# Optimization experiments

Measured on AMD Instinct MI355X. Metric: run time of the kernel, lower is better.

The kernel has to match this reference:

```python
import jax, jax.numpy as jnp
import numpy as np

EMB_DIM = 1024
K = 512
N = 65536
B = 128
EPS = 1e-8  # torch cosine_similarity eps


def setup_inputs() -> dict:
    key = jax.random.key(0)
    k1, k2, k3, k4 = jax.random.split(key, 4)
    x = jax.random.normal(k1, (B, K, EMB_DIM), dtype=jnp.float32)
    query = jax.random.normal(k2, (EMB_DIM,), dtype=jnp.float32)
    # learned parameters: N separate (1, emb_dim) params, concatenated -> [N, EMB_DIM]
    glorot_std = float(np.sqrt(6.0 / (1 + EMB_DIM)))
    prompts = jax.random.uniform(k3, (N, EMB_DIM), dtype=jnp.float32,
                                 minval=-glorot_std, maxval=glorot_std)
    keys = jax.random.normal(k4, (N, EMB_DIM), dtype=jnp.float32)
    return {"x": x, "query": query, "keys": keys, "prompts": prompts}


def reference(x, query, keys, prompts):
    # cosine similarity between query [D] and each key row [N, D]
    q_norm = jnp.maximum(jnp.linalg.norm(query), EPS)
    k_norms = jnp.maximum(jnp.linalg.norm(keys, axis=1), EPS)  # [N]
    sims = (keys @ query) / (k_norms * q_norm)                 # [N]
    _, topk_idx = jax.lax.top_k(sims, K)                       # [K]
    selected = prompts[topk_idx]                               # [K, D] gather
    return x + selected                                        # broadcast over batch
```

## Files before the change

kernel.cpp:

```cpp
#include <hip/hip_runtime.h>
#include <cfloat>
#include <cstdint>

#define EMB_DIM 1024
#define NKEYS   65536
#define TOPK    512
#define BATCH   128
#define NBINS   4096
#define CAP     2048

__global__ __launch_bounds__(256) void sims_kernel(
    const float* __restrict__ keys, const float* __restrict__ query,
    double* __restrict__ sims)
{
    const int wave = threadIdx.x >> 6;
    const int lane = threadIdx.x & 63;
    const int row  = blockIdx.x * 4 + wave;

    const float4* __restrict__ krow = (const float4*)(keys + (size_t)row * EMB_DIM);
    const float4* __restrict__ q4   = (const float4*)query;

    double dot = 0.0, ss = 0.0;
#pragma unroll
    for (int j = 0; j < 4; ++j) {
        const int c = lane + 64 * j;
        float4 kv = krow[c];
        float4 qv = q4[c];
        dot += (double)kv.x * qv.x + (double)kv.y * qv.y +
               (double)kv.z * qv.z + (double)kv.w * qv.w;
        ss  += (double)kv.x * kv.x + (double)kv.y * kv.y +
               (double)kv.z * kv.z + (double)kv.w * kv.w;
    }
#pragma unroll
    for (int off = 32; off > 0; off >>= 1) {
        dot += __shfl_xor(dot, off);
        ss  += __shfl_xor(ss, off);
    }
    if (lane == 0) {
        double norm = sqrt(ss);
        if (norm < 1e-8) norm = 1e-8;
        sims[row] = dot / norm;
    }
}

__device__ __forceinline__ unsigned mono32(float f) {
    unsigned u = __float_as_uint(f);
    return (u & 0x80000000u) ? ~u : (u | 0x80000000u);
}

__global__ __launch_bounds__(1024) void topk_kernel(
    const double* __restrict__ sims, int* __restrict__ topk)
{
    __shared__ int    hist[NBINS];
    __shared__ int    sfx[NBINS];
    __shared__ double cs[CAP];
    __shared__ int    ci[CAP];
    __shared__ int    bstar_s;
    __shared__ int    cnt;

    const int tid = threadIdx.x;

    for (int i = tid; i < NBINS; i += 1024) hist[i] = 0;
    if (tid == 0) cnt = 0;
    __syncthreads();

    for (int n = tid; n < NKEYS; n += 1024) {
        unsigned b = mono32((float)sims[n]) >> 20;
        atomicAdd(&hist[b], 1);
    }
    __syncthreads();

    int* src = hist;
    int* dst = sfx;
    for (int off = 1; off < NBINS; off <<= 1) {
        for (int i = tid; i < NBINS; i += 1024) {
            int v = src[i];
            if (i + off < NBINS) v += src[i + off];
            dst[i] = v;
        }
        __syncthreads();
        int* t = src; src = dst; dst = t;
    }
    for (int i = tid; i < NBINS; i += 1024) {
        if (src[i] >= TOPK && (i == NBINS - 1 || src[i + 1] < TOPK)) bstar_s = i;
    }
    __syncthreads();
    const int bstar = bstar_s;

    for (int n = tid; n < NKEYS; n += 1024) {
        double s = sims[n];
        unsigned b = mono32((float)s) >> 20;
        if ((int)b >= bstar) {
            int pos = atomicAdd(&cnt, 1);
            if (pos < CAP) { cs[pos] = s; ci[pos] = n; }
        }
    }
    __syncthreads();

    int c = cnt; if (c > CAP) c = CAP;
    for (int i = tid; i < CAP; i += 1024) {
        if (i >= c) { cs[i] = -DBL_MAX; ci[i] = 0x7fffffff; }
    }
    __syncthreads();

    for (int k = 2; k <= CAP; k <<= 1) {
        for (int j = k >> 1; j > 0; j >>= 1) {
            for (int i = tid; i < CAP; i += 1024) {
                int ixj = i ^ j;
                if (ixj > i) {
                    double s1 = cs[i], s2 = cs[ixj];
                    int    i1 = ci[i], i2 = ci[ixj];
                    bool a_after_b = (s1 < s2) || (s1 == s2 && i1 > i2);
                    bool up = ((i & k) == 0);
                    if (up ? a_after_b : !a_after_b) {
                        cs[i] = s2; ci[i] = i2;
                        cs[ixj] = s1; ci[ixj] = i1;
                    }
                }
            }
            __syncthreads();
        }
    }

    if (tid < TOPK) topk[tid] = ci[tid];
}

__global__ __launch_bounds__(256) void add_kernel(
    const float* __restrict__ x, const float* __restrict__ prompts,
    const int* __restrict__ topk, float* __restrict__ out)
{
    const int b = blockIdx.x & (BATCH - 1);
    const int k = blockIdx.x >> 7;
    const int idx = topk[k];

    const size_t row = ((size_t)b * TOPK + k) * (EMB_DIM / 4);
    const float4* __restrict__ xr = (const float4*)x + row;
    const float4* __restrict__ pr = (const float4*)prompts + (size_t)idx * (EMB_DIM / 4);
    float4* __restrict__ outr = (float4*)out + row;

    const int t = threadIdx.x;
    float4 xv = xr[t];
    float4 pv = pr[t];
    outr[t] = make_float4(xv.x + pv.x, xv.y + pv.y, xv.z + pv.z, xv.w + pv.w);
}

extern "C" void kernel_launch(void* const* d_in, const int* in_sizes, int n_in,
                              void* d_out, int out_size, void* d_ws, size_t ws_size,
                              hipStream_t stream)
{
    const float* x       = (const float*)d_in[0];
    const float* query   = (const float*)d_in[1];
    const float* keys    = (const float*)d_in[2];
    const float* prompts = (const float*)d_in[3];

    double* sims = (double*)d_ws;
    int*    topk = (int*)((char*)d_ws + NKEYS * sizeof(double));

    sims_kernel<<<NKEYS / 4, 256, 0, stream>>>(keys, query, sims);
    topk_kernel<<<1, 1024, 0, stream>>>(sims, topk);
    add_kernel<<<BATCH * TOPK, 256, 0, stream>>>(x, prompts, topk, (float*)d_out);
}
```

Before: 763.1 us.

## Split single-block top-k into fused histogram, parallel collect, and rank-based selection

Builds the similarity histogram with global atomics inside the sims kernel instead of a second pass in a single block. The threshold bin is found in a small kernel, candidate collection runs across 64 blocks, and the bitonic sort is replaced by an O(c^2) rank count that writes each winner directly to its position. This targets the serial single-block top-k stage, at the cost of more kernel launches, global atomic contention on the histogram, and quadratic work in the candidate count.

```diff
diff --git a/kernel.cpp b/kernel.cpp
--- a/kernel.cpp
+++ b/kernel.cpp
@@ -9,9 +9,21 @@
 #define NBINS   4096
 #define CAP     2048
 
+__device__ __forceinline__ unsigned mono32(float f) {
+    unsigned u = __float_as_uint(f);
+    return (u & 0x80000000u) ? ~u : (u | 0x80000000u);
+}
+
+__global__ __launch_bounds__(1024) void init_kernel(int* __restrict__ hist)
+{
+#pragma unroll
+    for (int j = 0; j < NBINS / 1024; ++j) hist[threadIdx.x + 1024 * j] = 0;
+    if (threadIdx.x == 0) hist[NBINS] = 0;
+}
+
 __global__ __launch_bounds__(256) void sims_kernel(
     const float* __restrict__ keys, const float* __restrict__ query,
-    double* __restrict__ sims)
+    double* __restrict__ sims, int* __restrict__ hist)
 {
     const int wave = threadIdx.x >> 6;
     const int lane = threadIdx.x & 63;
@@ -39,39 +51,24 @@
     if (lane == 0) {
         double norm = sqrt(ss);
         if (norm < 1e-8) norm = 1e-8;
-        sims[row] = dot / norm;
+        double s = dot / norm;
+        sims[row] = s;
+        atomicAdd(&hist[mono32((float)s) >> 20], 1);
     }
 }
 
-__device__ __forceinline__ unsigned mono32(float f) {
-    unsigned u = __float_as_uint(f);
-    return (u & 0x80000000u) ? ~u : (u | 0x80000000u);
-}
-
-__global__ __launch_bounds__(1024) void topk_kernel(
-    const double* __restrict__ sims, int* __restrict__ topk)
+__global__ __launch_bounds__(1024) void bstar_kernel(
+    const int* __restrict__ hist_g, int* __restrict__ bstar_g)
 {
-    __shared__ int    hist[NBINS];
-    __shared__ int    sfx[NBINS];
-    __shared__ double cs[CAP];
-    __shared__ int    ci[CAP];
-    __shared__ int    bstar_s;
-    __shared__ int    cnt;
-
+    __shared__ int h[NBINS];
+    __shared__ int s2[NBINS];
     const int tid = threadIdx.x;
 
-    for (int i = tid; i < NBINS; i += 1024) hist[i] = 0;
-    if (tid == 0) cnt = 0;
+    for (int i = tid; i < NBINS; i += 1024) h[i] = hist_g[i];
     __syncthreads();
 
-    for (int n = tid; n < NKEYS; n += 1024) {
-        unsigned b = mono32((float)sims[n]) >> 20;
-        atomicAdd(&hist[b], 1);
-    }
-    __syncthreads();
-
-    int* src = hist;
-    int* dst = sfx;
+    int* src = h;
+    int* dst = s2;
     for (int off = 1; off < NBINS; off <<= 1) {
         for (int i = tid; i < NBINS; i += 1024) {
             int v = src[i];
@@ -82,47 +79,48 @@
         int* t = src; src = dst; dst = t;
     }
     for (int i = tid; i < NBINS; i += 1024) {
-        if (src[i] >= TOPK && (i == NBINS - 1 || src[i + 1] < TOPK)) bstar_s = i;
+        if (src[i] >= TOPK && (i == NBINS - 1 || src[i + 1] < TOPK)) *bstar_g = i;
     }
-    __syncthreads();
-    const int bstar = bstar_s;
+}
 
-    for (int n = tid; n < NKEYS; n += 1024) {
-        double s = sims[n];
-        unsigned b = mono32((float)s) >> 20;
-        if ((int)b >= bstar) {
-            int pos = atomicAdd(&cnt, 1);
-            if (pos < CAP) { cs[pos] = s; ci[pos] = n; }
-        }
+__global__ __launch_bounds__(1024) void collect_kernel(
+    const double* __restrict__ sims, const int* __restrict__ bstar_g,
+    int* __restrict__ cnt, double* __restrict__ cand_s, int* __restrict__ cand_i)
+{
+    const int n = blockIdx.x * 1024 + threadIdx.x;
+    const int bstar = *bstar_g;
+    double s = sims[n];
+    unsigned b = mono32((float)s) >> 20;
+    if ((int)b >= bstar) {
+        int pos = atomicAdd(cnt, 1);
+        if (pos < CAP) { cand_s[pos] = s; cand_i[pos] = n; }
     }
+}
+
+__global__ __launch_bounds__(1024) void rank_kernel(
+    const int* __restrict__ cnt_g, const double* __restrict__ cand_s,
+    const int* __restrict__ cand_i, int* __restrict__ topk)
+{
+    __shared__ double cs[CAP];
+    __shared__ int    ci[CAP];
+    const int tid = threadIdx.x;
+
+    int c = *cnt_g;
+    if (c > CAP) c = CAP;
+
+    for (int i = tid; i < c; i += 1024) { cs[i] = cand_s[i]; ci[i] = cand_i[i]; }
     __syncthreads();
 
-    int c = cnt; if (c > CAP) c = CAP;
-    for (int i = tid; i < CAP; i += 1024) {
-        if (i >= c) { cs[i] = -DBL_MAX; ci[i] = 0x7fffffff; }
+    for (int i = tid; i < c; i += 1024) {
+        const double s  = cs[i];
+        const int    id = ci[i];
+        int rank = 0;
+        for (int j = 0; j < c; ++j) {
+            double sj = cs[j];
+            rank += (sj > s || (sj == s && ci[j] < id)) ? 1 : 0;
+        }
+        if (rank < TOPK) topk[rank] = id;
     }
-    __syncthreads();
-
-    for (int k = 2; k <= CAP; k <<= 1) {
-        for (int j = k >> 1; j > 0; j >>= 1) {
-            for (int i = tid; i < CAP; i += 1024) {
-                int ixj = i ^ j;
-                if (ixj > i) {
-                    double s1 = cs[i], s2 = cs[ixj];
-                    int    i1 = ci[i], i2 = ci[ixj];
-                    bool a_after_b = (s1 < s2) || (s1 == s2 && i1 > i2);
-                    bool up = ((i & k) == 0);
-                    if (up ? a_after_b : !a_after_b) {
-                        cs[i] = s2; ci[i] = i2;
-                        cs[ixj] = s1; ci[ixj] = i1;
-                    }
-                }
-            }
-            __syncthreads();
-        }
-    }
-
-    if (tid < TOPK) topk[tid] = ci[tid];
 }
 
 __global__ __launch_bounds__(256) void add_kernel(
@@ -153,10 +151,19 @@
     const float* keys    = (const float*)d_in[2];
     const float* prompts = (const float*)d_in[3];
 
-    double* sims = (double*)d_ws;
-    int*    topk = (int*)((char*)d_ws + NKEYS * sizeof(double));
+    char* w = (char*)d_ws;
+    double* sims   = (double*)(w);
+    int*    topk   = (int*)(w + 524288);
+    int*    hist   = (int*)(w + 526336);
+    int*    cnt    = hist + NBINS;
+    int*    bstar  = hist + NBINS + 1;
+    double* cand_s = (double*)(w + 542736);
+    int*    cand_i = (int*)(w + 542736 + CAP * 8);
 
-    sims_kernel<<<NKEYS / 4, 256, 0, stream>>>(keys, query, sims);
-    topk_kernel<<<1, 1024, 0, stream>>>(sims, topk);
-    add_kernel<<<BATCH * TOPK, 256, 0, stream>>>(x, prompts, topk, (float*)d_out);
+    init_kernel   <<<1, 1024, 0, stream>>>(hist);
+    sims_kernel   <<<NKEYS / 4, 256, 0, stream>>>(keys, query, sims, hist);
+    bstar_kernel  <<<1, 1024, 0, stream>>>(hist, bstar);
+    collect_kernel<<<NKEYS / 1024, 1024, 0, stream>>>(sims, bstar, cnt, cand_s, cand_i);
+    rank_kernel   <<<1, 1024, 0, stream>>>(cnt, cand_s, cand_i, topk);
+    add_kernel    <<<BATCH * TOPK, 256, 0, stream>>>(x, prompts, topk, (float*)d_out);
 }
```

Result: slower. 885.0 us (+16.0%).
